# Performance work log

Hardware: AMD Instinct MI355X
Metric: run time of the kernel (lower is better)

Reference implementation:

```python
import jax, jax.numpy as jnp
import numpy as np

NL, D, DI, N, R, K = 4, 256, 512, 16, 16, 4  # layers, d_model, d_inner, d_state, dt_rank, conv kernel


def setup_inputs() -> dict:
    key = jax.random.key(0)
    ks = jax.random.split(key, 10)
    b, nc, nt = 8, 256, 64
    xc = jax.random.normal(ks[0], (b, nc, D), jnp.float32)
    xt = jax.random.normal(ks[1], (b, nt, D), jnp.float32)
    ln_g = jnp.ones((NL, D), jnp.float32)
    ln_b = jnp.zeros((NL, D), jnp.float32)
    W_in = jax.random.normal(ks[2], (NL, D, 2 * DI), jnp.float32) * (D ** -0.5)
    W_conv = jax.random.normal(ks[3], (NL, DI, 1, K), jnp.float32) * 0.2
    b_conv = jnp.zeros((NL, DI), jnp.float32)
    W_x = jax.random.normal(ks[4], (NL, DI, R + 2 * N), jnp.float32) * (DI ** -0.5)
    W_dt = jax.random.normal(ks[5], (NL, R, DI), jnp.float32) * (R ** -0.5)
    b_dt = jax.random.normal(ks[6], (NL, DI), jnp.float32) * 0.5 - 4.0  # softplus ~ 0.02
    A_log = jnp.broadcast_to(jnp.log(jnp.arange(1, N + 1, dtype=jnp.float32)), (NL, DI, N)).copy()
    Dp = jnp.ones((NL, DI), jnp.float32)
    W_out = jax.random.normal(ks[7], (NL, DI, D), jnp.float32) * (DI ** -0.5)
    return dict(xc=xc, xt=xt, ln_g=ln_g, ln_b=ln_b, W_in=W_in, W_conv=W_conv, b_conv=b_conv,
                W_x=W_x, W_dt=W_dt, b_dt=b_dt, A_log=A_log, Dp=Dp, W_out=W_out)


def _mamba_layer(x, g, beta, Wi, Wc, bc, Wx, Wdt, bdt, Alog, Dvec, Wo):
    # x: [B, L, D]; pre-LN residual Mamba-1 block
    mu = jnp.mean(x, axis=-1, keepdims=True)
    var = jnp.var(x, axis=-1, keepdims=True)
    h = (x - mu) * jax.lax.rsqrt(var + 1e-5) * g + beta
    xz = h @ Wi                              # [B, L, 2*DI]
    xp, z = xz[..., :DI], xz[..., DI:]
    # causal depthwise conv1d
    xcv = jax.lax.conv_general_dilated(xp.transpose(0, 2, 1), Wc, (1,), [(K - 1, 0)],
                                       feature_group_count=DI,
                                       dimension_numbers=('NCH', 'OIH', 'NCH'))
    xcv = jax.nn.silu(xcv.transpose(0, 2, 1) + bc)  # [B, L, DI]
    dbl = xcv @ Wx                           # [B, L, R+2N]
    dt = jax.nn.softplus(dbl[..., :R] @ Wdt + bdt)   # [B, L, DI]
    Bm = dbl[..., R:R + N]                   # [B, L, N]
    Cm = dbl[..., R + N:]                    # [B, L, N]
    A = -jnp.exp(Alog)                       # [DI, N]

    def step(hst, inp):
        x_t, dt_t, b_t, c_t = inp            # [B,DI],[B,DI],[B,N],[B,N]
        dA = jnp.exp(dt_t[:, :, None] * A)   # [B, DI, N]
        hst = dA * hst + (dt_t * x_t)[:, :, None] * b_t[:, None, :]
        return hst, jnp.einsum('bdn,bn->bd', hst, c_t)

    h0 = jnp.zeros((x.shape[0], DI, N), x.dtype)
    _, ys = jax.lax.scan(step, h0, (xcv.transpose(1, 0, 2), dt.transpose(1, 0, 2),
                                    Bm.transpose(1, 0, 2), Cm.transpose(1, 0, 2)))
    y = ys.transpose(1, 0, 2) + xcv * Dvec
    y = y * jax.nn.silu(z)
    return x + y @ Wo


def reference(xc, xt, ln_g, ln_b, W_in, W_conv, b_conv, W_x, W_dt, b_dt, A_log, Dp, W_out):
    b, nc, d = xc.shape
    nt = xt.shape[1]
    # replicate context per target token: [b*nt, nc+1, d]
    xr = jnp.broadcast_to(xc[:, None], (b, nt, nc, d)).reshape(b * nt, nc, d)
    x = jnp.concatenate([xr, xt.reshape(b * nt, 1, d)], axis=1)
    for i in range(NL):
        x = _mamba_layer(x, ln_g[i], ln_b[i], W_in[i], W_conv[i], b_conv[i],
                         W_x[i], W_dt[i], b_dt[i], A_log[i], Dp[i], W_out[i])
    return x[:, -1, :].reshape(b, nt, d)
```

## Files before the change

### kernel.cpp

```cpp
#include <hip/hip_runtime.h>
#include <hip/hip_bf16.h>

#define D_     256
#define TWO_DI 1024
#define DI_    512
#define NSTATE 16
#define RR     16
#define NDBL   48
#define BSEQ   8
#define NC     256
#define NCHUNK 16
#define CLEN   16
#define CTX    2048
#define TGT    512

typedef __attribute__((ext_vector_type(8))) short short8v;
typedef __attribute__((ext_vector_type(8))) unsigned short ushort8v;
typedef __attribute__((ext_vector_type(4))) float floatx4;

__device__ __forceinline__ float siluf(float x) { return x / (1.f + __expf(-x)); }
__device__ __forceinline__ float softplusf(float x) {
  return fmaxf(x, 0.f) + log1pf(__expf(-fabsf(x)));
}
__device__ __forceinline__ unsigned short f2bf(float x) {
  unsigned u = __float_as_uint(x);
  u += 0x7fffu + ((u >> 16) & 1u);
  return (unsigned short)(u >> 16);
}
__device__ __forceinline__ float bf2f(unsigned short b) {
  return __uint_as_float((unsigned)b << 16);
}

__global__ __launch_bounds__(256) void prep_all(
    const float* __restrict__ W_in, const float* __restrict__ W_o,
    const float* __restrict__ W_x, const float* __restrict__ Alog,
    const float* __restrict__ W_dt,
    unsigned short* __restrict__ Wint, unsigned short* __restrict__ Wot,
    unsigned short* __restrict__ Wxt, float* __restrict__ Aneg,
    float* __restrict__ WdtT)
{
  __shared__ float tile[32][33];
  int b = blockIdx.x;
  const float* src; unsigned short* dst; int R, C, cx, ry;
  if (b < 1024) {
    int z = b >> 8, t = b & 255; cx = t & 31; ry = t >> 5; R = 256; C = 1024;
    src = W_in + (size_t)z * R * C; dst = Wint + (size_t)z * R * C;
  } else if (b < 1536) {
    int bb = b - 1024; int z = bb >> 7, t = bb & 127; cx = t & 7; ry = t >> 3; R = 512; C = 256;
    src = W_o + (size_t)z * R * C; dst = Wot + (size_t)z * R * C;
  } else if (b < 1664) {
    int bb = b - 1536; int z = bb >> 5, t = bb & 31; cx = t & 1; ry = t >> 1; R = 512; C = 48;
    src = W_x + (size_t)z * R * C; dst = Wxt + (size_t)z * R * C;
  } else if (b < 1792) {
    int i = (b - 1664) * 256 + threadIdx.x;
    if (i < 4 * DI_ * NSTATE) Aneg[i] = -__expf(Alog[i]);
    return;
  } else {
    int i = (b - 1792) * 256 + threadIdx.x;
    int z = i >> 13, rem = i & 8191, c = rem >> 4, r = rem & 15;
    WdtT[i] = W_dt[(size_t)z * RR * DI_ + r * DI_ + c];
    return;
  }
  int c0 = cx * 32, r0 = ry * 32;
  int tx = threadIdx.x & 31, ty = threadIdx.x >> 5;
#pragma unroll
  for (int i = 0; i < 4; ++i) {
    int r = r0 + ty + i * 8;
    tile[ty + i * 8][tx] = (r < R && c0 + tx < C) ? src[(size_t)r * C + c0 + tx] : 0.f;
  }
  __syncthreads();
#pragma unroll
  for (int i = 0; i < 4; ++i) {
    int c = c0 + ty + i * 8;
    if (c < C && r0 + tx < R)
      dst[(size_t)c * R + r0 + tx] = f2bf(tile[tx][ty + i * 8]);
  }
}

template<int EPI>
__device__ __forceinline__ void gemm_in_ln_body(
    unsigned short (*As)[72], unsigned short (*Bs)[72],
    float* gs, float* bs, int bx, int by,
    const float* __restrict__ X, const float* __restrict__ g,
    const float* __restrict__ be, const unsigned short* __restrict__ Bt,
    float* __restrict__ C, int N,
    const float* __restrict__ cconv, const float* __restrict__ Wc4,
    unsigned short* __restrict__ xcv_bf, float* __restrict__ zbuf)
{
  const int K = D_;
  int tid = threadIdx.x;
  int n0 = bx * 64, m0 = by * 64;
  int w = tid >> 6, lane = tid & 63;
  int lr = lane & 15, kq = lane >> 4;
  int wr = w >> 1, wc = w & 1;
  int srow = tid >> 2, schunk = (tid & 3) * 16;
  const float* Apf = &X[(size_t)(m0 + srow) * K];
  {
    const float4* xr = reinterpret_cast<const float4*>(&Apf[(tid & 3) * 64]);
    float s = 0.f, sq = 0.f;
#pragma unroll
    for (int i = 0; i < 16; ++i) {
      float4 v = xr[i];
      s += v.x + v.y + v.z + v.w;
      sq += v.x * v.x + v.y * v.y + v.z * v.z + v.w * v.w;
    }
    s += __shfl_xor(s, 1);  s += __shfl_xor(s, 2);
    sq += __shfl_xor(sq, 1); sq += __shfl_xor(sq, 2);
    float mu = s * (1.f / K);
    float rstd = rsqrtf(sq * (1.f / K) - mu * mu + 1e-5f);
    gs[tid] = g[tid]; bs[tid] = be[tid];
    const unsigned short* Bp = &Bt[(size_t)(n0 + srow) * K + schunk];
    float4 af[4];
#pragma unroll
    for (int i = 0; i < 4; ++i)
      af[i] = *reinterpret_cast<const float4*>(&Apf[schunk + i * 4]);
    ushort8v b0 = *reinterpret_cast<const ushort8v*>(Bp);
    ushort8v b1 = *reinterpret_cast<const ushort8v*>(Bp + 8);
    floatx4 acc[2][2] = {};
    for (int k0 = 0; k0 < K; k0 += 64) {
      __syncthreads();
      {
        int cb = k0 + schunk;
        ushort8v o0, o1;
#pragma unroll
        for (int i = 0; i < 4; ++i) {
          float4 v = af[i];
          unsigned short e0 = f2bf((v.x - mu) * rstd * gs[cb + i * 4 + 0] + bs[cb + i * 4 + 0]);
          unsigned short e1 = f2bf((v.y - mu) * rstd * gs[cb + i * 4 + 1] + bs[cb + i * 4 + 1]);
          unsigned short e2 = f2bf((v.z - mu) * rstd * gs[cb + i * 4 + 2] + bs[cb + i * 4 + 2]);
          unsigned short e3 = f2bf((v.w - mu) * rstd * gs[cb + i * 4 + 3] + bs[cb + i * 4 + 3]);
          if (i < 2) { o0[i*4] = (short)e0; o0[i*4+1] = (short)e1; o0[i*4+2] = (short)e2; o0[i*4+3] = (short)e3; }
          else { int j = (i-2)*4; o1[j] = (short)e0; o1[j+1] = (short)e1; o1[j+2] = (short)e2; o1[j+3] = (short)e3; }
        }
        *reinterpret_cast<ushort8v*>(&As[srow][schunk])     = o0;
        *reinterpret_cast<ushort8v*>(&As[srow][schunk + 8]) = o1;
      }
      *reinterpret_cast<ushort8v*>(&Bs[srow][schunk])     = b0;
      *reinterpret_cast<ushort8v*>(&Bs[srow][schunk + 8]) = b1;
      __syncthreads();
      if (k0 + 64 < K) {
#pragma unroll
        for (int i = 0; i < 4; ++i)
          af[i] = *reinterpret_cast<const float4*>(&Apf[k0 + 64 + schunk + i * 4]);
        b0 = *reinterpret_cast<const ushort8v*>(Bp + k0 + 64);
        b1 = *reinterpret_cast<const ushort8v*>(Bp + k0 + 72);
      }
#pragma unroll
      for (int ks = 0; ks < 2; ++ks) {
        short8v af2[2], bf2v[2];
#pragma unroll
        for (int f = 0; f < 2; ++f)
          af2[f] = *reinterpret_cast<const short8v*>(&As[wr * 32 + f * 16 + lr][ks * 32 + kq * 8]);
#pragma unroll
        for (int g2 = 0; g2 < 2; ++g2)
          bf2v[g2] = *reinterpret_cast<const short8v*>(&Bs[wc * 32 + g2 * 16 + lr][ks * 32 + kq * 8]);
#pragma unroll
        for (int f = 0; f < 2; ++f)
#pragma unroll
          for (int g2 = 0; g2 < 2; ++g2)
            acc[f][g2] = __builtin_amdgcn_mfma_f32_16x16x32_bf16(af2[f], bf2v[g2], acc[f][g2], 0, 0, 0);
      }
    }
#pragma unroll
    for (int f = 0; f < 2; ++f)
#pragma unroll
      for (int g2 = 0; g2 < 2; ++g2) {
        int col = n0 + wc * 32 + g2 * 16 + lr;
#pragma unroll
        for (int r = 0; r < 4; ++r) {
          int row = m0 + wr * 32 + f * 16 + kq * 4 + r;
          float v = acc[f][g2][r];
          if (EPI == 0) {
            C[(size_t)row * N + col] = v;
          } else {
            int bb = row >> 6;
            if (col < DI_) {
              float sv = siluf(cconv[bb * DI_ + col] + v * Wc4[col * 4 + 3]);
              xcv_bf[(size_t)row * DI_ + col] = f2bf(sv);
            } else {
              zbuf[(size_t)row * DI_ + (col - DI_)] = v;
            }
          }
        }
      }
  }
}

template<int EPI>
__global__ __launch_bounds__(256) void gemm_in_ln(
    const float* __restrict__ X, const float* __restrict__ g,
    const float* __restrict__ be, const unsigned short* __restrict__ Bt,
    float* __restrict__ C,
    const float* __restrict__ cconv, const float* __restrict__ Wc4,
    unsigned short* __restrict__ xcv_bf, float* __restrict__ zbuf)
{
  __shared__ unsigned short As[64][72];
  __shared__ unsigned short Bs[64][72];
  __shared__ float gs[256], bs[256];
  gemm_in_ln_body<EPI>(As, Bs, gs, bs, blockIdx.x, blockIdx.y, X, g, be, Bt,
                       C, TWO_DI, cconv, Wc4, xcv_bf, zbuf);
}

__global__ __launch_bounds__(256) void fused_gemm_in_ln(
    const float* __restrict__ Xa, const float* __restrict__ ga,
    const float* __restrict__ ba, float* __restrict__ Ca,
    const unsigned short* __restrict__ Bta,
    const float* __restrict__ Xb, const float* __restrict__ gb,
    const float* __restrict__ bb, const unsigned short* __restrict__ Btb,
    const float* __restrict__ cconv, const float* __restrict__ Wc4,
    unsigned short* __restrict__ xcv_bf, float* __restrict__ zbuf)
{
  __shared__ unsigned short As[64][72];
  __shared__ unsigned short Bs[64][72];
  __shared__ float gs[256], bs[256];
  int f = blockIdx.x;
  if (f < 512)
    gemm_in_ln_body<0>(As, Bs, gs, bs, f & 15, f >> 4, Xa, ga, ba, Bta,
                       Ca, TWO_DI, nullptr, nullptr, nullptr, nullptr);
  else {
    f -= 512;
    gemm_in_ln_body<1>(As, Bs, gs, bs, f & 15, f >> 4, Xb, gb, bb, Btb,
                       nullptr, TWO_DI, cconv, Wc4, xcv_bf, zbuf);
  }
}

__global__ __launch_bounds__(256) void gemm_out(
    const unsigned short* __restrict__ A, const unsigned short* __restrict__ Bt,
    const float* __restrict__ resid, float* __restrict__ C, int N, int K)
{
  __shared__ unsigned short As[64][72];
  __shared__ unsigned short Bs[64][72];
  int tid = threadIdx.x;
  int n0 = blockIdx.x * 64, m0 = blockIdx.y * 64;
  int w = tid >> 6, lane = tid & 63;
  int lr = lane & 15, kq = lane >> 4;
  int wr = w >> 1, wc = w & 1;
  int srow = tid >> 2, schunk = (tid & 3) * 16;
  const unsigned short* Ap = &A[(size_t)(m0 + srow) * K + schunk];
  const unsigned short* Bp = &Bt[(size_t)(n0 + srow) * K + schunk];
  ushort8v a0 = *reinterpret_cast<const ushort8v*>(Ap);
  ushort8v a1 = *reinterpret_cast<const ushort8v*>(Ap + 8);
  ushort8v b0 = *reinterpret_cast<const ushort8v*>(Bp);
  ushort8v b1 = *reinterpret_cast<const ushort8v*>(Bp + 8);
  floatx4 acc[2][2] = {};
  for (int k0 = 0; k0 < K; k0 += 64) {
    __syncthreads();
    *reinterpret_cast<ushort8v*>(&As[srow][schunk])     = a0;
    *reinterpret_cast<ushort8v*>(&As[srow][schunk + 8]) = a1;
    *reinterpret_cast<ushort8v*>(&Bs[srow][schunk])     = b0;
    *reinterpret_cast<ushort8v*>(&Bs[srow][schunk + 8]) = b1;
    __syncthreads();
    if (k0 + 64 < K) {
      a0 = *reinterpret_cast<const ushort8v*>(Ap + k0 + 64);
      a1 = *reinterpret_cast<const ushort8v*>(Ap + k0 + 72);
      b0 = *reinterpret_cast<const ushort8v*>(Bp + k0 + 64);
      b1 = *reinterpret_cast<const ushort8v*>(Bp + k0 + 72);
    }
#pragma unroll
    for (int ks = 0; ks < 2; ++ks) {
      short8v af[2], bf2v[2];
#pragma unroll
      for (int f = 0; f < 2; ++f)
        af[f] = *reinterpret_cast<const short8v*>(&As[wr * 32 + f * 16 + lr][ks * 32 + kq * 8]);
#pragma unroll
      for (int g2 = 0; g2 < 2; ++g2)
        bf2v[g2] = *reinterpret_cast<const short8v*>(&Bs[wc * 32 + g2 * 16 + lr][ks * 32 + kq * 8]);
#pragma unroll
      for (int f = 0; f < 2; ++f)
#pragma unroll
        for (int g2 = 0; g2 < 2; ++g2)
          acc[f][g2] = __builtin_amdgcn_mfma_f32_16x16x32_bf16(af[f], bf2v[g2], acc[f][g2], 0, 0, 0);
    }
  }
#pragma unroll
  for (int f = 0; f < 2; ++f)
#pragma unroll
    for (int g2 = 0; g2 < 2; ++g2) {
      int col = n0 + wc * 32 + g2 * 16 + lr;
#pragma unroll
      for (int r = 0; r < 4; ++r) {
        int row = m0 + wr * 32 + f * 16 + kq * 4 + r;
        float v = acc[f][g2][r] + resid[(size_t)row * N + col];
        C[(size_t)row * N + col] = v;
      }
    }
}

__device__ __forceinline__ void gemm_s_body(int bx, int by,
    const unsigned short* __restrict__ A, const unsigned short* __restrict__ Bt,
    const float* __restrict__ resid, float* __restrict__ C, int N, int K)
{
  __shared__ unsigned short As[32][72];
  __shared__ unsigned short Bs[32][72];
  int tid = threadIdx.x;
  int n0 = bx * 32, m0 = by * 32;
  int w = tid >> 6, lane = tid & 63;
  int lr = lane & 15, kq = lane >> 4;
  int wr = w >> 1, wc = w & 1;
  int srow = tid >> 3, schunk = (tid & 7) * 8;
  const unsigned short* Ap = &A[(size_t)(m0 + srow) * K + schunk];
  const unsigned short* Bp = &Bt[(size_t)(n0 + srow) * K + schunk];
  ushort8v a0 = *reinterpret_cast<const ushort8v*>(Ap);
  ushort8v b0 = *reinterpret_cast<const ushort8v*>(Bp);
  floatx4 acc = {};
  for (int k0 = 0; k0 < K; k0 += 64) {
    __syncthreads();
    *reinterpret_cast<ushort8v*>(&As[srow][schunk]) = a0;
    *reinterpret_cast<ushort8v*>(&Bs[srow][schunk]) = b0;
    __syncthreads();
    if (k0 + 64 < K) {
      a0 = *reinterpret_cast<const ushort8v*>(Ap + k0 + 64);
      b0 = *reinterpret_cast<const ushort8v*>(Bp + k0 + 64);
    }
#pragma unroll
    for (int ks = 0; ks < 2; ++ks) {
      short8v af = *reinterpret_cast<const short8v*>(&As[wr * 16 + lr][ks * 32 + kq * 8]);
      short8v bf = *reinterpret_cast<const short8v*>(&Bs[wc * 16 + lr][ks * 32 + kq * 8]);
      acc = __builtin_amdgcn_mfma_f32_16x16x32_bf16(af, bf, acc, 0, 0, 0);
    }
  }
  int col = n0 + wc * 16 + lr;
#pragma unroll
  for (int r = 0; r < 4; ++r) {
    int row = m0 + wr * 16 + kq * 4 + r;
    float v = acc[r] + resid[(size_t)row * N + col];
    C[(size_t)row * N + col] = v;
  }
}

__global__ __launch_bounds__(256) void gemm_s(
    const unsigned short* __restrict__ A, const unsigned short* __restrict__ Bt,
    const float* __restrict__ resid, float* __restrict__ C, int N, int K)
{
  gemm_s_body(blockIdx.x, blockIdx.y, A, Bt, resid, C, N, K);
}

__device__ __forceinline__ void conv_body_lean(int blk,
    const float* __restrict__ xz, const float* __restrict__ Wc,
    const float* __restrict__ bc, const unsigned short* __restrict__ Wxt,
    const float* __restrict__ WdtT, const float* __restrict__ bdt,
    unsigned short* __restrict__ xcvb, float* __restrict__ dtb,
    float* __restrict__ dblg, float* __restrict__ cconv)
{
  __shared__ unsigned short xcs[16][528];
  __shared__ float dbl_s[16][48];
  int seq = blk >> 4, ch = blk & 15;
  int tok0 = blk * 16;
  int tid = threadIdx.x;
  int base = ch * 16;
#pragma unroll
  for (int hh = 0; hh < 2; ++hh) {
    int c = tid + hh * 256;
    const float4 wv = *reinterpret_cast<const float4*>(&Wc[c * 4]);
    float bcv = bc[c];
    const float* xzs = &xz[(size_t)(seq * NC) * TWO_DI + c];
    float r[19];
#pragma unroll
    for (int i = 0; i < 19; ++i) {
      int tl = base - 3 + i;
      r[i] = (tl >= 0) ? xzs[(size_t)tl * TWO_DI] : 0.f;
    }
#pragma unroll
    for (int t = 0; t < 16; ++t) {
      float acc = bcv + r[t] * wv.x + r[t + 1] * wv.y + r[t + 2] * wv.z + r[t + 3] * wv.w;
      unsigned short sv = f2bf(siluf(acc));
      xcs[t][c] = sv;
      xcvb[(size_t)(tok0 + t) * DI_ + c] = sv;
    }
    if (ch == 15)
      cconv[seq * DI_ + c] = bcv + r[16] * wv.x + r[17] * wv.y + r[18] * wv.z;
  }
  __syncthreads();
  int w = tid >> 6, lane = tid & 63, lr = lane & 15, kq = lane >> 4;
  if (w < 3) {
    floatx4 acc = {};
#pragma unroll
    for (int kc = 0; kc < 16; ++kc) {
      short8v bb = *reinterpret_cast<const short8v*>(&Wxt[(size_t)(w * 16 + lr) * DI_ + kc * 32 + kq * 8]);
      short8v aa = *reinterpret_cast<const short8v*>(&xcs[lr][kc * 32 + kq * 8]);
      acc = __builtin_amdgcn_mfma_f32_16x16x32_bf16(aa, bb, acc, 0, 0, 0);
    }
#pragma unroll
    for (int r2 = 0; r2 < 4; ++r2) {
      int t = kq * 4 + r2, col = w * 16 + lr;
      dbl_s[t][col] = acc[r2];
      dblg[(size_t)(tok0 + t) * NDBL + col] = acc[r2];
    }
  }
  __syncthreads();
#pragma unroll
  for (int hh = 0; hh < 2; ++hh) {
    int c = tid + hh * 256;
    float wr_[16];
    const float4* wt4 = reinterpret_cast<const float4*>(&WdtT[c * 16]);
#pragma unroll
    for (int q = 0; q < 4; ++q) {
      float4 v4 = wt4[q];
      wr_[q * 4] = v4.x; wr_[q * 4 + 1] = v4.y; wr_[q * 4 + 2] = v4.z; wr_[q * 4 + 3] = v4.w;
    }
    float bv = bdt[c];
#pragma unroll
    for (int t = 0; t < 16; ++t) {
      float accd = bv;
#pragma unroll
      for (int r2 = 0; r2 < 16; ++r2) accd += dbl_s[t][r2] * wr_[r2];
      dtb[(size_t)(tok0 + t) * DI_ + c] = softplusf(accd);
    }
  }
}

__global__ __launch_bounds__(256) void conv_lean_kern(
    const float* __restrict__ xz, const float* __restrict__ Wc,
    const float* __restrict__ bc, const unsigned short* __restrict__ Wxt,
    const float* __restrict__ WdtT, const float* __restrict__ bdt,
    unsigned short* __restrict__ xcvb, float* __restrict__ dtb,
    float* __restrict__ dblg, float* __restrict__ cconv)
{
  conv_body_lean(blockIdx.x, xz, Wc, bc, Wxt, WdtT, bdt, xcvb, dtb, dblg, cconv);
}

__device__ __forceinline__ void sp_body(int b,
    const float* __restrict__ dblg, const unsigned short* __restrict__ xcvb,
    const float* __restrict__ dtb, const float* __restrict__ Aneg,
    float* __restrict__ Sb, float* __restrict__ Pb)
{
  int dg = b & 31, sc = b >> 5;
  int tid = threadIdx.x;
  int tt = tid >> 4, cc = tid & 15;
  int tok0 = sc * CLEN;
  __shared__ float dts[16][17], xs[16][17], Bsh[16][17];
  dts[tt][cc] = dtb[(size_t)(tok0 + tt) * DI_ + dg * 16 + cc];
  xs[tt][cc]  = bf2f(xcvb[(size_t)(tok0 + tt) * DI_ + dg * 16 + cc]);
  Bsh[tt][cc] = dblg[(size_t)(tok0 + tt) * NDBL + RR + cc];
  __syncthreads();
  int dl = tt, n = cc;
  int d = dg * 16 + dl;
  float A = Aneg[d * NSTATE + n];
  float Bn[16];
#pragma unroll
  for (int t = 0; t < CLEN; ++t) Bn[t] = Bsh[t][n];
  float h = 0.f, p = 1.f;
#pragma unroll
  for (int t = 0; t < CLEN; ++t) {
    float dtv = dts[t][dl];
    float dA  = __expf(dtv * A);
    h = fmaf(dA, h, dtv * xs[t][dl] * Bn[t]);
    p *= dA;
  }
  size_t o = ((size_t)sc * DI_ + d) * NSTATE + n;
  Sb[o] = h; Pb[o] = p;
}

__global__ __launch_bounds__(256) void sp_kern(
    const float* __restrict__ dblg, const unsigned short* __restrict__ xcvb,
    const float* __restrict__ dtb, const float* __restrict__ Aneg,
    float* __restrict__ Sb, float* __restrict__ Pb)
{
  sp_body(blockIdx.x, dblg, xcvb, dtb, Aneg, Sb, Pb);
}

__global__ __launch_bounds__(256) void fused_sp_gout(
    const unsigned short* __restrict__ Ag, const unsigned short* __restrict__ Btg,
    const float* __restrict__ residg, float* __restrict__ Cg,
    const float* __restrict__ dblg, const unsigned short* __restrict__ xcvb,
    const float* __restrict__ dtb, const float* __restrict__ Aneg,
    float* __restrict__ Sb, float* __restrict__ Pb)
{
  if (blockIdx.x < 128) {
    int f = blockIdx.x;
    gemm_s_body(f & 7, f >> 3, Ag, Btg, residg, Cg, D_, DI_);
  } else {
    sp_body(blockIdx.x - 128, dblg, xcvb, dtb, Aneg, Sb, Pb);
  }
}

__global__ __launch_bounds__(256) void scan_fin(
    const float* __restrict__ dblg, const unsigned short* __restrict__ xcvb,
    const float* __restrict__ xz, const float* __restrict__ dtb,
    const float* __restrict__ Sb, const float* __restrict__ Pb,
    const float* __restrict__ Aneg, const float* __restrict__ Dp,
    unsigned short* __restrict__ yb, float* __restrict__ hstate)
{
  int b = blockIdx.x;
  int dg = b & 31, sc = b >> 5;
  int seq = sc >> 4, chunk = sc & 15;
  int tid = threadIdx.x;
  int tt = tid >> 4, cc = tid & 15;
  int tok0 = sc * CLEN;
  __shared__ float dts[16][17], xs[16][17], zs[16][17], Bsh[16][17], Csh[16][17], ys[16][17];
  dts[tt][cc] = dtb[(size_t)(tok0 + tt) * DI_ + dg * 16 + cc];
  xs[tt][cc]  = bf2f(xcvb[(size_t)(tok0 + tt) * DI_ + dg * 16 + cc]);
  zs[tt][cc]  = xz[(size_t)(tok0 + tt) * TWO_DI + DI_ + dg * 16 + cc];
  Bsh[tt][cc] = dblg[(size_t)(tok0 + tt) * NDBL + RR + cc];
  Csh[tt][cc] = dblg[(size_t)(tok0 + tt) * NDBL + RR + NSTATE + cc];
  __syncthreads();
  int dl = tt, n = cc;
  int d = dg * 16 + dl;
  float A  = Aneg[d * NSTATE + n];
  float Dv = Dp[d];
  float Bn[16], Cn[16];
#pragma unroll
  for (int t = 0; t < CLEN; ++t) { Bn[t] = Bsh[t][n]; Cn[t] = Csh[t][n]; }
  float h = 0.f;
  for (int c2 = 0; c2 < chunk; ++c2) {
    size_t o = ((size_t)(seq * NCHUNK + c2) * DI_ + d) * NSTATE + n;
    h = fmaf(Pb[o], h, Sb[o]);
  }
#pragma unroll
  for (int t = 0; t < CLEN; ++t) {
    float dtv = dts[t][dl];
    float xv  = xs[t][dl];
    float dA  = __expf(dtv * A);
    h = fmaf(dA, h, dtv * xv * Bn[t]);
    float p = h * Cn[t];
    p += __shfl_xor(p, 1); p += __shfl_xor(p, 2);
    p += __shfl_xor(p, 4); p += __shfl_xor(p, 8);
    if (n == 0) ys[t][dl] = (p + xv * Dv) * siluf(zs[t][dl]);
  }
  __syncthreads();
  yb[(size_t)(tok0 + tt) * DI_ + dg * 16 + cc] = f2bf(ys[tt][cc]);
  if (chunk == NCHUNK - 1)
    hstate[(size_t)seq * DI_ * NSTATE + d * NSTATE + n] = h;
}

__device__ __forceinline__ void ssm_body(int blk,
    const unsigned short* __restrict__ xcv_bf, const float* __restrict__ zbuf,
    const unsigned short* __restrict__ Wx, const float* __restrict__ WdtT_l,
    const float* __restrict__ bdt_l, const float* __restrict__ An_l,
    const float* __restrict__ Dp_l, const float* __restrict__ hs,
    unsigned short* __restrict__ ybf)
{
  __shared__ float dbl_s[16][48];
  int tg = blk >> 3, cg = blk & 7;
  int tok0 = tg * 16;
  int b = tg >> 2;
  int tid = threadIdx.x;
  int w = tid >> 6, lane = tid & 63, lr = lane & 15, kq = lane >> 4;
  if (w < 3) {
    floatx4 acc = {};
#pragma unroll
    for (int kc = 0; kc < 16; ++kc) {
      short8v bb = *reinterpret_cast<const short8v*>(&Wx[(size_t)(w * 16 + lr) * DI_ + kc * 32 + kq * 8]);
      short8v aa = *reinterpret_cast<const short8v*>(&xcv_bf[(size_t)(tok0 + lr) * DI_ + kc * 32 + kq * 8]);
      acc = __builtin_amdgcn_mfma_f32_16x16x32_bf16(aa, bb, acc, 0, 0, 0);
    }
#pragma unroll
    for (int r = 0; r < 4; ++r)
      dbl_s[kq * 4 + r][w * 16 + lr] = acc[r];
  }
  __syncthreads();
  int c = cg * 64 + (tid & 63);
  int t0 = (tid >> 6) * 4;
  float wdt_r[16], An[16], hr[16];
  const float4* wt4 = reinterpret_cast<const float4*>(&WdtT_l[c * 16]);
  const float4* An4 = reinterpret_cast<const float4*>(&An_l[c * NSTATE]);
  const float4* hr4 = reinterpret_cast<const float4*>(&hs[(size_t)b * DI_ * NSTATE + c * NSTATE]);
#pragma unroll
  for (int q = 0; q < 4; ++q) {
    float4 wv = wt4[q]; wdt_r[q*4]=wv.x; wdt_r[q*4+1]=wv.y; wdt_r[q*4+2]=wv.z; wdt_r[q*4+3]=wv.w;
    float4 a = An4[q]; An[q*4]=a.x; An[q*4+1]=a.y; An[q*4+2]=a.z; An[q*4+3]=a.w;
    float4 hv = hr4[q]; hr[q*4]=hv.x; hr[q*4+1]=hv.y; hr[q*4+2]=hv.z; hr[q*4+3]=hv.w;
  }
  float Dv = Dp_l[c], bv = bdt_l[c];
#pragma unroll
  for (int tt = 0; tt < 4; ++tt) {
    int t = t0 + tt;
    float accd = bv;
#pragma unroll
    for (int r = 0; r < 16; ++r) accd += dbl_s[t][r] * wdt_r[r];
    float dtv = softplusf(accd);
    float xv = bf2f(xcv_bf[(size_t)(tok0 + t) * DI_ + c]);
    float coef = dtv * xv;
    float y = 0.f;
#pragma unroll
    for (int n = 0; n < 16; ++n) {
      float hn = fmaf(__expf(dtv * An[n]), hr[n], coef * dbl_s[t][RR + n]);
      y = fmaf(hn, dbl_s[t][RR + NSTATE + n], y);
    }
    float yv = (y + xv * Dv) * siluf(zbuf[(size_t)(tok0 + t) * DI_ + c]);
    ybf[(size_t)(tok0 + t) * DI_ + c] = f2bf(yv);
  }
}

__global__ __launch_bounds__(256) void tgt_ssm2(
    const unsigned short* __restrict__ xcv_bf, const float* __restrict__ zbuf,
    const unsigned short* __restrict__ Wx, const float* __restrict__ WdtT_l,
    const float* __restrict__ bdt_l, const float* __restrict__ An_l,
    const float* __restrict__ Dp_l, const float* __restrict__ hs,
    unsigned short* __restrict__ ybf)
{
  ssm_body(blockIdx.x, xcv_bf, zbuf, Wx, WdtT_l, bdt_l, An_l, Dp_l, hs, ybf);
}

__global__ __launch_bounds__(256) void fused_conv_ssm(
    const float* __restrict__ xz, const float* __restrict__ Wc,
    const float* __restrict__ bc, const unsigned short* __restrict__ WxtA,
    const float* __restrict__ WdtTA, const float* __restrict__ bdtA,
    unsigned short* __restrict__ xcvb, float* __restrict__ dtb,
    float* __restrict__ dblg, float* __restrict__ cconv,
    const unsigned short* __restrict__ xcv_bfB, const float* __restrict__ zbufB,
    const unsigned short* __restrict__ WxB, const float* __restrict__ WdtTB,
    const float* __restrict__ bdtB, const float* __restrict__ AnB,
    const float* __restrict__ DpB, const float* __restrict__ hsB,
    unsigned short* __restrict__ ybfB)
{
  if (blockIdx.x < BSEQ * NCHUNK)
    conv_body_lean(blockIdx.x, xz, Wc, bc, WxtA, WdtTA, bdtA,
                   xcvb, dtb, dblg, cconv);
  else
    ssm_body(blockIdx.x - BSEQ * NCHUNK, xcv_bfB, zbufB, WxB, WdtTB, bdtB,
             AnB, DpB, hsB, ybfB);
}

extern "C" void kernel_launch(void* const* d_in, const int* in_sizes, int n_in,
                              void* d_out, int out_size, void* d_ws, size_t ws_size,
                              hipStream_t stream)
{
  const float* xc   = (const float*)d_in[0];
  const float* xt   = (const float*)d_in[1];
  const float* ln_g = (const float*)d_in[2];
  const float* ln_b = (const float*)d_in[3];
  const float* W_in = (const float*)d_in[4];
  const float* W_cv = (const float*)d_in[5];
  const float* b_cv = (const float*)d_in[6];
  const float* W_x  = (const float*)d_in[7];
  const float* W_dt = (const float*)d_in[8];
  const float* b_dt = (const float*)d_in[9];
  const float* Alog = (const float*)d_in[10];
  const float* Dp   = (const float*)d_in[11];
  const float* W_o  = (const float*)d_in[12];
  float* out = (float*)d_out;

  float* ws = (float*)d_ws;
  size_t off = 0;
  auto alloc = [&](size_t n) { float* p = ws + off; off += n; return p; };
  float* xz     = alloc((size_t)CTX * TWO_DI);
  float* dtb    = alloc((size_t)CTX * DI_);
  float* dblg   = alloc((size_t)CTX * NDBL);
  float* xcur   = alloc((size_t)CTX * D_);
  float* Sb     = alloc((size_t)BSEQ * NCHUNK * DI_ * NSTATE);
  float* Pb     = alloc((size_t)BSEQ * NCHUNK * DI_ * NSTATE);
  float* cconvT = alloc((size_t)4 * BSEQ * DI_);
  float* hst    = alloc((size_t)4 * BSEQ * DI_ * NSTATE);
  float* Aneg   = alloc((size_t)4 * DI_ * NSTATE);
  float* WdtT   = alloc((size_t)4 * DI_ * RR);
  float* zbufB  = alloc((size_t)TGT * DI_);
  float* xtb    = alloc((size_t)TGT * D_);
  unsigned short* xcvb    = (unsigned short*)alloc((size_t)CTX * DI_ / 2);
  unsigned short* yb_bf   = (unsigned short*)alloc((size_t)CTX * DI_ / 2);
  unsigned short* xcv_bfB = (unsigned short*)alloc((size_t)TGT * DI_ / 2);
  unsigned short* y_bfB   = (unsigned short*)alloc((size_t)TGT * DI_ / 2);
  unsigned short* Wint    = (unsigned short*)alloc((size_t)4 * TWO_DI * D_ / 2);
  unsigned short* Wot     = (unsigned short*)alloc((size_t)4 * D_ * DI_ / 2);
  unsigned short* Wxt     = (unsigned short*)alloc((size_t)4 * NDBL * DI_ / 2);
  if (off * sizeof(float) > ws_size) return;

  prep_all<<<1920, 256, 0, stream>>>(W_in, W_o, W_x, Alog, W_dt,
                                     Wint, Wot, Wxt, Aneg, WdtT);

  gemm_in_ln<0><<<dim3(16, CTX / 64), 256, 0, stream>>>(
      xc, ln_g, ln_b, Wint, xz, nullptr, nullptr, nullptr, nullptr);
  conv_lean_kern<<<BSEQ * NCHUNK, 256, 0, stream>>>(
      xz, W_cv, b_cv, Wxt, WdtT, b_dt, xcvb, dtb, dblg, cconvT);
  sp_kern<<<BSEQ * NCHUNK * 32, 256, 0, stream>>>(dblg, xcvb, dtb, Aneg, Sb, Pb);
  scan_fin<<<BSEQ * NCHUNK * 32, 256, 0, stream>>>(
      dblg, xcvb, xz, dtb, Sb, Pb, Aneg, Dp, yb_bf, hst);
  gemm_out<<<dim3(D_ / 64, CTX / 64), 256, 0, stream>>>(
      yb_bf, Wot, xc, xcur, D_, DI_);

  for (int l = 0; l < 3; ++l) {
    int la = l + 1;
    const float* xinB = (l == 0) ? xt : xtb;
    fused_gemm_in_ln<<<512 + 128, 256, 0, stream>>>(
        xcur, ln_g + la * D_, ln_b + la * D_, xz, Wint + (size_t)la * TWO_DI * D_,
        xinB, ln_g + l * D_, ln_b + l * D_, Wint + (size_t)l * TWO_DI * D_,
        cconvT + (size_t)l * BSEQ * DI_, W_cv + l * DI_ * 4, xcv_bfB, zbufB);
    fused_conv_ssm<<<BSEQ * NCHUNK + 256, 256, 0, stream>>>(
        xz, W_cv + la * DI_ * 4, b_cv + la * DI_, Wxt + (size_t)la * NDBL * DI_,
        WdtT + (size_t)la * DI_ * RR, b_dt + la * DI_,
        xcvb, dtb, dblg, cconvT + (size_t)la * BSEQ * DI_,
        xcv_bfB, zbufB, Wxt + (size_t)l * NDBL * DI_, WdtT + (size_t)l * DI_ * RR,
        b_dt + l * DI_, Aneg + l * DI_ * NSTATE, Dp + l * DI_,
        hst + (size_t)l * BSEQ * DI_ * NSTATE, y_bfB);
    fused_sp_gout<<<128 + BSEQ * NCHUNK * 32, 256, 0, stream>>>(
        y_bfB, Wot + (size_t)l * D_ * DI_, xinB, xtb,
        dblg, xcvb, dtb, Aneg + la * DI_ * NSTATE, Sb, Pb);
    scan_fin<<<BSEQ * NCHUNK * 32, 256, 0, stream>>>(
        dblg, xcvb, xz, dtb, Sb, Pb, Aneg + la * DI_ * NSTATE, Dp + la * DI_,
        yb_bf, hst + (size_t)la * BSEQ * DI_ * NSTATE);
    if (la < 3)
      gemm_out<<<dim3(D_ / 64, CTX / 64), 256, 0, stream>>>(
          yb_bf, Wot + (size_t)la * D_ * DI_, xcur, xcur, D_, DI_);
  }

  gemm_in_ln<1><<<dim3(16, TGT / 64), 256, 0, stream>>>(
      xtb, ln_g + 3 * D_, ln_b + 3 * D_, Wint + (size_t)3 * TWO_DI * D_, nullptr,
      cconvT + (size_t)3 * BSEQ * DI_, W_cv + 3 * DI_ * 4, xcv_bfB, zbufB);
  tgt_ssm2<<<256, 256, 0, stream>>>(xcv_bfB, zbufB,
      Wxt + (size_t)3 * NDBL * DI_, WdtT + (size_t)3 * DI_ * RR, b_dt + 3 * DI_,
      Aneg + 3 * DI_ * NSTATE, Dp + 3 * DI_,
      hst + (size_t)3 * BSEQ * DI_ * NSTATE, y_bfB);
  gemm_s<<<dim3(D_ / 32, TGT / 32), 256, 0, stream>>>(
      y_bfB, Wot + (size_t)3 * D_ * DI_, xtb, out, D_, DI_);
}
```

Before: 316.7 us.

## Fold LayerNorm into W_in and fuse chunk-scan partials into conv kernel

Folds the LayerNorm gain into the bf16 W_in weights during prep and precomputes per-column weight sums and bias projections. The input GEMM can then feed raw x as bf16 and apply the mean and rstd correction in the epilogue. The chunk-local scan (S/P partials) moves into the conv kernel, which removes the separate sp kernel and its reload of dt, x and B. The layer loop merges scan_fin with the output GEMM to save a launch. The cost is atomics in prep and a different bf16 rounding point: raw x is quantised before centring, which can lose precision when the row mean is large relative to the spread.

```diff
diff --git a/kernel.cpp b/kernel.cpp
--- a/kernel.cpp
+++ b/kernel.cpp
@@ -35,17 +35,48 @@
     const float* __restrict__ W_in, const float* __restrict__ W_o,
     const float* __restrict__ W_x, const float* __restrict__ Alog,
     const float* __restrict__ W_dt,
+    const float* __restrict__ ln_g, const float* __restrict__ ln_b,
     unsigned short* __restrict__ Wint, unsigned short* __restrict__ Wot,
     unsigned short* __restrict__ Wxt, float* __restrict__ Aneg,
-    float* __restrict__ WdtT)
+    float* __restrict__ WdtT, float* __restrict__ cs0, float* __restrict__ bW)
 {
   __shared__ float tile[32][33];
   int b = blockIdx.x;
+  int tx = threadIdx.x & 31, ty = threadIdx.x >> 5;
+  if (b < 1024) {
+    int z = b >> 8, t = b & 255; int cx = t & 31, ry = t >> 5;
+    const int R = 256, C = 1024;
+    const float* src = W_in + (size_t)z * R * C;
+    unsigned short* dst = Wint + (size_t)z * R * C;
+    int c0 = cx * 32, r0 = ry * 32;
+#pragma unroll
+    for (int i = 0; i < 4; ++i)
+      tile[ty + i * 8][tx] = src[(size_t)(r0 + ty + i * 8) * C + c0 + tx];
+    __syncthreads();
+    float gv  = ln_g[z * D_ + r0 + tx];
+    float bev = ln_b[z * D_ + r0 + tx];
+#pragma unroll
+    for (int i = 0; i < 4; ++i) {
+      int c = c0 + ty + i * 8;
+      float wv = tile[tx][ty + i * 8];
+      unsigned short h = f2bf(wv * gv);
+      dst[(size_t)c * R + r0 + tx] = h;
+      float cs = bf2f(h);
+      float bs = bev * wv;
+#pragma unroll
+      for (int off = 1; off <= 16; off <<= 1) {
+        cs += __shfl_xor(cs, off);
+        bs += __shfl_xor(bs, off);
+      }
+      if (tx == 0) {
+        atomicAdd(&cs0[z * TWO_DI + c], cs);
+        atomicAdd(&bW[z * TWO_DI + c], bs);
+      }
+    }
+    return;
+  }
   const float* src; unsigned short* dst; int R, C, cx, ry;
-  if (b < 1024) {
-    int z = b >> 8, t = b & 255; cx = t & 31; ry = t >> 5; R = 256; C = 1024;
-    src = W_in + (size_t)z * R * C; dst = Wint + (size_t)z * R * C;
-  } else if (b < 1536) {
+  if (b < 1536) {
     int bb = b - 1024; int z = bb >> 7, t = bb & 127; cx = t & 7; ry = t >> 3; R = 512; C = 256;
     src = W_o + (size_t)z * R * C; dst = Wot + (size_t)z * R * C;
   } else if (b < 1664) {
@@ -62,7 +93,6 @@
     return;
   }
   int c0 = cx * 32, r0 = ry * 32;
-  int tx = threadIdx.x & 31, ty = threadIdx.x >> 5;
 #pragma unroll
   for (int i = 0; i < 4; ++i) {
     int r = r0 + ty + i * 8;
@@ -80,147 +110,144 @@
 template<int EPI>
 __device__ __forceinline__ void gemm_in_ln_body(
     unsigned short (*As)[72], unsigned short (*Bs)[72],
-    float* gs, float* bs, int bx, int by,
-    const float* __restrict__ X, const float* __restrict__ g,
-    const float* __restrict__ be, const unsigned short* __restrict__ Bt,
-    float* __restrict__ C, int N,
+    float* mus, float* rstds, int bx, int by,
+    const float* __restrict__ X, const unsigned short* __restrict__ Bt,
+    const float* __restrict__ cs0, const float* __restrict__ bW,
+    float* __restrict__ C,
     const float* __restrict__ cconv, const float* __restrict__ Wc4,
     unsigned short* __restrict__ xcv_bf, float* __restrict__ zbuf)
 {
-  const int K = D_;
+  const int K = D_, N = TWO_DI;
   int tid = threadIdx.x;
   int n0 = bx * 64, m0 = by * 64;
   int w = tid >> 6, lane = tid & 63;
   int lr = lane & 15, kq = lane >> 4;
   int wr = w >> 1, wc = w & 1;
-  int srow = tid >> 2, schunk = (tid & 3) * 16;
+  int srow = tid >> 2, q = tid & 3, schunk = q * 16;
   const float* Apf = &X[(size_t)(m0 + srow) * K];
-  {
-    const float4* xr = reinterpret_cast<const float4*>(&Apf[(tid & 3) * 64]);
-    float s = 0.f, sq = 0.f;
-#pragma unroll
-    for (int i = 0; i < 16; ++i) {
-      float4 v = xr[i];
-      s += v.x + v.y + v.z + v.w;
+  float4 xr[4][4];
+#pragma unroll
+  for (int j = 0; j < 4; ++j)
+#pragma unroll
+    for (int i = 0; i < 4; ++i)
+      xr[j][i] = *reinterpret_cast<const float4*>(&Apf[j * 64 + schunk + i * 4]);
+  float s = 0.f, sq = 0.f;
+#pragma unroll
+  for (int j = 0; j < 4; ++j)
+#pragma unroll
+    for (int i = 0; i < 4; ++i) {
+      float4 v = xr[j][i];
+      s  += v.x + v.y + v.z + v.w;
       sq += v.x * v.x + v.y * v.y + v.z * v.z + v.w * v.w;
     }
-    s += __shfl_xor(s, 1);  s += __shfl_xor(s, 2);
-    sq += __shfl_xor(sq, 1); sq += __shfl_xor(sq, 2);
-    float mu = s * (1.f / K);
-    float rstd = rsqrtf(sq * (1.f / K) - mu * mu + 1e-5f);
-    gs[tid] = g[tid]; bs[tid] = be[tid];
-    const unsigned short* Bp = &Bt[(size_t)(n0 + srow) * K + schunk];
-    float4 af[4];
-#pragma unroll
-    for (int i = 0; i < 4; ++i)
-      af[i] = *reinterpret_cast<const float4*>(&Apf[schunk + i * 4]);
-    ushort8v b0 = *reinterpret_cast<const ushort8v*>(Bp);
-    ushort8v b1 = *reinterpret_cast<const ushort8v*>(Bp + 8);
-    floatx4 acc[2][2] = {};
-    for (int k0 = 0; k0 < K; k0 += 64) {
-      __syncthreads();
-      {
-        int cb = k0 + schunk;
-        ushort8v o0, o1;
-#pragma unroll
-        for (int i = 0; i < 4; ++i) {
-          float4 v = af[i];
-          unsigned short e0 = f2bf((v.x - mu) * rstd * gs[cb + i * 4 + 0] + bs[cb + i * 4 + 0]);
-          unsigned short e1 = f2bf((v.y - mu) * rstd * gs[cb + i * 4 + 1] + bs[cb + i * 4 + 1]);
-          unsigned short e2 = f2bf((v.z - mu) * rstd * gs[cb + i * 4 + 2] + bs[cb + i * 4 + 2]);
-          unsigned short e3 = f2bf((v.w - mu) * rstd * gs[cb + i * 4 + 3] + bs[cb + i * 4 + 3]);
-          if (i < 2) { o0[i*4] = (short)e0; o0[i*4+1] = (short)e1; o0[i*4+2] = (short)e2; o0[i*4+3] = (short)e3; }
-          else { int j = (i-2)*4; o1[j] = (short)e0; o1[j+1] = (short)e1; o1[j+2] = (short)e2; o1[j+3] = (short)e3; }
-        }
-        *reinterpret_cast<ushort8v*>(&As[srow][schunk])     = o0;
-        *reinterpret_cast<ushort8v*>(&As[srow][schunk + 8]) = o1;
+  s += __shfl_xor(s, 1);  s += __shfl_xor(s, 2);
+  sq += __shfl_xor(sq, 1); sq += __shfl_xor(sq, 2);
+  float mu   = s * (1.f / K);
+  float rstd = rsqrtf(sq * (1.f / K) - mu * mu + 1e-5f);
+  if (q == 0) { mus[srow] = mu; rstds[srow] = rstd; }
+  const unsigned short* Bp = &Bt[(size_t)(n0 + srow) * K + schunk];
+  ushort8v b0 = *reinterpret_cast<const ushort8v*>(Bp);
+  ushort8v b1 = *reinterpret_cast<const ushort8v*>(Bp + 8);
+  floatx4 acc[2][2] = {};
+#pragma unroll
+  for (int j = 0; j < 4; ++j) {
+    __syncthreads();
+    {
+      ushort8v o0, o1;
+#pragma unroll
+      for (int i = 0; i < 4; ++i) {
+        float4 v = xr[j][i];
+        unsigned short e0 = f2bf(v.x), e1 = f2bf(v.y), e2 = f2bf(v.z), e3 = f2bf(v.w);
+        if (i < 2) { o0[i*4] = (short)e0; o0[i*4+1] = (short)e1; o0[i*4+2] = (short)e2; o0[i*4+3] = (short)e3; }
+        else { int jj = (i - 2) * 4; o1[jj] = (short)e0; o1[jj+1] = (short)e1; o1[jj+2] = (short)e2; o1[jj+3] = (short)e3; }
       }
-      *reinterpret_cast<ushort8v*>(&Bs[srow][schunk])     = b0;
-      *reinterpret_cast<ushort8v*>(&Bs[srow][schunk + 8]) = b1;
-      __syncthreads();
-      if (k0 + 64 < K) {
-#pragma unroll
-        for (int i = 0; i < 4; ++i)
-          af[i] = *reinterpret_cast<const float4*>(&Apf[k0 + 64 + schunk + i * 4]);
-        b0 = *reinterpret_cast<const ushort8v*>(Bp + k0 + 64);
-        b1 = *reinterpret_cast<const ushort8v*>(Bp + k0 + 72);
-      }
-#pragma unroll
-      for (int ks = 0; ks < 2; ++ks) {
-        short8v af2[2], bf2v[2];
-#pragma unroll
-        for (int f = 0; f < 2; ++f)
-          af2[f] = *reinterpret_cast<const short8v*>(&As[wr * 32 + f * 16 + lr][ks * 32 + kq * 8]);
+      *reinterpret_cast<ushort8v*>(&As[srow][schunk])     = o0;
+      *reinterpret_cast<ushort8v*>(&As[srow][schunk + 8]) = o1;
+    }
+    *reinterpret_cast<ushort8v*>(&Bs[srow][schunk])     = b0;
+    *reinterpret_cast<ushort8v*>(&Bs[srow][schunk + 8]) = b1;
+    __syncthreads();
+    if (j < 3) {
+      b0 = *reinterpret_cast<const ushort8v*>(Bp + j * 64 + 64);
+      b1 = *reinterpret_cast<const ushort8v*>(Bp + j * 64 + 72);
+    }
+#pragma unroll
+    for (int ks = 0; ks < 2; ++ks) {
+      short8v af2[2], bf2v[2];
+#pragma unroll
+      for (int f = 0; f < 2; ++f)
+        af2[f] = *reinterpret_cast<const short8v*>(&As[wr * 32 + f * 16 + lr][ks * 32 + kq * 8]);
+#pragma unroll
+      for (int g2 = 0; g2 < 2; ++g2)
+        bf2v[g2] = *reinterpret_cast<const short8v*>(&Bs[wc * 32 + g2 * 16 + lr][ks * 32 + kq * 8]);
+#pragma unroll
+      for (int f = 0; f < 2; ++f)
 #pragma unroll
         for (int g2 = 0; g2 < 2; ++g2)
-          bf2v[g2] = *reinterpret_cast<const short8v*>(&Bs[wc * 32 + g2 * 16 + lr][ks * 32 + kq * 8]);
-#pragma unroll
-        for (int f = 0; f < 2; ++f)
-#pragma unroll
-          for (int g2 = 0; g2 < 2; ++g2)
-            acc[f][g2] = __builtin_amdgcn_mfma_f32_16x16x32_bf16(af2[f], bf2v[g2], acc[f][g2], 0, 0, 0);
-      }
-    }
-#pragma unroll
-    for (int f = 0; f < 2; ++f)
-#pragma unroll
-      for (int g2 = 0; g2 < 2; ++g2) {
-        int col = n0 + wc * 32 + g2 * 16 + lr;
-#pragma unroll
-        for (int r = 0; r < 4; ++r) {
-          int row = m0 + wr * 32 + f * 16 + kq * 4 + r;
-          float v = acc[f][g2][r];
-          if (EPI == 0) {
-            C[(size_t)row * N + col] = v;
+          acc[f][g2] = __builtin_amdgcn_mfma_f32_16x16x32_bf16(af2[f], bf2v[g2], acc[f][g2], 0, 0, 0);
+    }
+  }
+#pragma unroll
+  for (int f = 0; f < 2; ++f)
+#pragma unroll
+    for (int g2 = 0; g2 < 2; ++g2) {
+      int col = n0 + wc * 32 + g2 * 16 + lr;
+      float c0v = cs0[col], bwv = bW[col];
+#pragma unroll
+      for (int r = 0; r < 4; ++r) {
+        int rowl = wr * 32 + f * 16 + kq * 4 + r;
+        int row  = m0 + rowl;
+        float v = rstds[rowl] * (acc[f][g2][r] - mus[rowl] * c0v) + bwv;
+        if (EPI == 0) {
+          C[(size_t)row * N + col] = v;
+        } else {
+          int bb = row >> 6;
+          if (col < DI_) {
+            float sv = siluf(cconv[bb * DI_ + col] + v * Wc4[col * 4 + 3]);
+            xcv_bf[(size_t)row * DI_ + col] = f2bf(sv);
           } else {
-            int bb = row >> 6;
-            if (col < DI_) {
-              float sv = siluf(cconv[bb * DI_ + col] + v * Wc4[col * 4 + 3]);
-              xcv_bf[(size_t)row * DI_ + col] = f2bf(sv);
-            } else {
-              zbuf[(size_t)row * DI_ + (col - DI_)] = v;
-            }
+            zbuf[(size_t)row * DI_ + (col - DI_)] = v;
           }
         }
       }
-  }
+    }
 }
 
 template<int EPI>
 __global__ __launch_bounds__(256) void gemm_in_ln(
-    const float* __restrict__ X, const float* __restrict__ g,
-    const float* __restrict__ be, const unsigned short* __restrict__ Bt,
+    const float* __restrict__ X, const unsigned short* __restrict__ Bt,
+    const float* __restrict__ cs0, const float* __restrict__ bW,
     float* __restrict__ C,
     const float* __restrict__ cconv, const float* __restrict__ Wc4,
     unsigned short* __restrict__ xcv_bf, float* __restrict__ zbuf)
 {
   __shared__ unsigned short As[64][72];
   __shared__ unsigned short Bs[64][72];
-  __shared__ float gs[256], bs[256];
-  gemm_in_ln_body<EPI>(As, Bs, gs, bs, blockIdx.x, blockIdx.y, X, g, be, Bt,
-                       C, TWO_DI, cconv, Wc4, xcv_bf, zbuf);
+  __shared__ float mus[64], rstds[64];
+  gemm_in_ln_body<EPI>(As, Bs, mus, rstds, blockIdx.x, blockIdx.y,
+                       X, Bt, cs0, bW, C, cconv, Wc4, xcv_bf, zbuf);
 }
 
 __global__ __launch_bounds__(256) void fused_gemm_in_ln(
-    const float* __restrict__ Xa, const float* __restrict__ ga,
-    const float* __restrict__ ba, float* __restrict__ Ca,
-    const unsigned short* __restrict__ Bta,
-    const float* __restrict__ Xb, const float* __restrict__ gb,
-    const float* __restrict__ bb, const unsigned short* __restrict__ Btb,
+    const float* __restrict__ Xa, const unsigned short* __restrict__ Bta,
+    const float* __restrict__ cs0a, const float* __restrict__ bWa,
+    float* __restrict__ Ca,
+    const float* __restrict__ Xb, const unsigned short* __restrict__ Btb,
+    const float* __restrict__ cs0b, const float* __restrict__ bWb,
     const float* __restrict__ cconv, const float* __restrict__ Wc4,
     unsigned short* __restrict__ xcv_bf, float* __restrict__ zbuf)
 {
   __shared__ unsigned short As[64][72];
   __shared__ unsigned short Bs[64][72];
-  __shared__ float gs[256], bs[256];
+  __shared__ float mus[64], rstds[64];
   int f = blockIdx.x;
   if (f < 512)
-    gemm_in_ln_body<0>(As, Bs, gs, bs, f & 15, f >> 4, Xa, ga, ba, Bta,
-                       Ca, TWO_DI, nullptr, nullptr, nullptr, nullptr);
+    gemm_in_ln_body<0>(As, Bs, mus, rstds, f & 15, f >> 4, Xa, Bta, cs0a, bWa,
+                       Ca, nullptr, nullptr, nullptr, nullptr);
   else {
     f -= 512;
-    gemm_in_ln_body<1>(As, Bs, gs, bs, f & 15, f >> 4, Xb, gb, bb, Btb,
-                       nullptr, TWO_DI, cconv, Wc4, xcv_bf, zbuf);
+    gemm_in_ln_body<1>(As, Bs, mus, rstds, f & 15, f >> 4, Xb, Btb, cs0b, bWb,
+                       nullptr, cconv, Wc4, xcv_bf, zbuf);
   }
 }
 
@@ -335,12 +362,14 @@
   gemm_s_body(blockIdx.x, blockIdx.y, A, Bt, resid, C, N, K);
 }
 
-__device__ __forceinline__ void conv_body_lean(int blk,
+__device__ __forceinline__ void conv_sp_body(int blk,
     const float* __restrict__ xz, const float* __restrict__ Wc,
     const float* __restrict__ bc, const unsigned short* __restrict__ Wxt,
     const float* __restrict__ WdtT, const float* __restrict__ bdt,
+    const float* __restrict__ Aneg,
     unsigned short* __restrict__ xcvb, float* __restrict__ dtb,
-    float* __restrict__ dblg, float* __restrict__ cconv)
+    float* __restrict__ dblg, float* __restrict__ cconv,
+    float* __restrict__ Sb, float* __restrict__ Pb)
 {
   __shared__ unsigned short xcs[16][528];
   __shared__ float dbl_s[16][48];
@@ -348,6 +377,7 @@
   int tok0 = blk * 16;
   int tid = threadIdx.x;
   int base = ch * 16;
+  float xv_t[2][16], dt_t[2][16];
 #pragma unroll
   for (int hh = 0; hh < 2; ++hh) {
     int c = tid + hh * 256;
@@ -362,10 +392,11 @@
     }
 #pragma unroll
     for (int t = 0; t < 16; ++t) {
-      float acc = bcv + r[t] * wv.x + r[t + 1] * wv.y + r[t + 2] * wv.z + r[t + 3] * wv.w;
-      unsigned short sv = f2bf(siluf(acc));
+      float a = bcv + r[t] * wv.x + r[t + 1] * wv.y + r[t + 2] * wv.z + r[t + 3] * wv.w;
+      unsigned short sv = f2bf(siluf(a));
       xcs[t][c] = sv;
       xcvb[(size_t)(tok0 + t) * DI_ + c] = sv;
+      xv_t[hh][t] = bf2f(sv);
     }
     if (ch == 15)
       cconv[seq * DI_ + c] = bcv + r[16] * wv.x + r[17] * wv.y + r[18] * wv.z;
@@ -394,9 +425,9 @@
     float wr_[16];
     const float4* wt4 = reinterpret_cast<const float4*>(&WdtT[c * 16]);
 #pragma unroll
-    for (int q = 0; q < 4; ++q) {
-      float4 v4 = wt4[q];
-      wr_[q * 4] = v4.x; wr_[q * 4 + 1] = v4.y; wr_[q * 4 + 2] = v4.z; wr_[q * 4 + 3] = v4.w;
+    for (int qq = 0; qq < 4; ++qq) {
+      float4 v4 = wt4[qq];
+      wr_[qq * 4] = v4.x; wr_[qq * 4 + 1] = v4.y; wr_[qq * 4 + 2] = v4.z; wr_[qq * 4 + 3] = v4.w;
     }
     float bv = bdt[c];
 #pragma unroll
@@ -404,84 +435,72 @@
       float accd = bv;
 #pragma unroll
       for (int r2 = 0; r2 < 16; ++r2) accd += dbl_s[t][r2] * wr_[r2];
-      dtb[(size_t)(tok0 + t) * DI_ + c] = softplusf(accd);
-    }
-  }
-}
-
-__global__ __launch_bounds__(256) void conv_lean_kern(
+      float dtv = softplusf(accd);
+      dt_t[hh][t] = dtv;
+      dtb[(size_t)(tok0 + t) * DI_ + c] = dtv;
+    }
+  }
+#pragma unroll
+  for (int hh = 0; hh < 2; ++hh) {
+    int d = tid + hh * 256;
+    float An[16];
+    const float4* An4 = reinterpret_cast<const float4*>(&Aneg[d * NSTATE]);
+#pragma unroll
+    for (int qq = 0; qq < 4; ++qq) {
+      float4 a = An4[qq];
+      An[qq * 4] = a.x; An[qq * 4 + 1] = a.y; An[qq * 4 + 2] = a.z; An[qq * 4 + 3] = a.w;
+    }
+    float h_n[16], p_n[16];
+#pragma unroll
+    for (int n = 0; n < 16; ++n) { h_n[n] = 0.f; p_n[n] = 1.f; }
+#pragma unroll
+    for (int t = 0; t < 16; ++t) {
+      float dtv  = dt_t[hh][t];
+      float coef = dtv * xv_t[hh][t];
+      float4 B0 = *reinterpret_cast<const float4*>(&dbl_s[t][RR]);
+      float4 B1 = *reinterpret_cast<const float4*>(&dbl_s[t][RR + 4]);
+      float4 B2 = *reinterpret_cast<const float4*>(&dbl_s[t][RR + 8]);
+      float4 B3 = *reinterpret_cast<const float4*>(&dbl_s[t][RR + 12]);
+      float Bv[16] = {B0.x, B0.y, B0.z, B0.w, B1.x, B1.y, B1.z, B1.w,
+                      B2.x, B2.y, B2.z, B2.w, B3.x, B3.y, B3.z, B3.w};
+#pragma unroll
+      for (int n = 0; n < 16; ++n) {
+        float dA = __expf(dtv * An[n]);
+        h_n[n] = fmaf(dA, h_n[n], coef * Bv[n]);
+        p_n[n] *= dA;
+      }
+    }
+    size_t ob = ((size_t)blk * DI_ + d) * NSTATE;
+#pragma unroll
+    for (int qq = 0; qq < 4; ++qq) {
+      *reinterpret_cast<float4*>(&Sb[ob + qq * 4]) =
+          make_float4(h_n[qq*4], h_n[qq*4+1], h_n[qq*4+2], h_n[qq*4+3]);
+      *reinterpret_cast<float4*>(&Pb[ob + qq * 4]) =
+          make_float4(p_n[qq*4], p_n[qq*4+1], p_n[qq*4+2], p_n[qq*4+3]);
+    }
+  }
+}
+
+__global__ __launch_bounds__(256) void conv_sp_kern(
     const float* __restrict__ xz, const float* __restrict__ Wc,
     const float* __restrict__ bc, const unsigned short* __restrict__ Wxt,
     const float* __restrict__ WdtT, const float* __restrict__ bdt,
+    const float* __restrict__ Aneg,
     unsigned short* __restrict__ xcvb, float* __restrict__ dtb,
-    float* __restrict__ dblg, float* __restrict__ cconv)
-{
-  conv_body_lean(blockIdx.x, xz, Wc, bc, Wxt, WdtT, bdt, xcvb, dtb, dblg, cconv);
-}
-
-__device__ __forceinline__ void sp_body(int b,
-    const float* __restrict__ dblg, const unsigned short* __restrict__ xcvb,
-    const float* __restrict__ dtb, const float* __restrict__ Aneg,
+    float* __restrict__ dblg, float* __restrict__ cconv,
     float* __restrict__ Sb, float* __restrict__ Pb)
 {
-  int dg = b & 31, sc = b >> 5;
-  int tid = threadIdx.x;
-  int tt = tid >> 4, cc = tid & 15;
-  int tok0 = sc * CLEN;
-  __shared__ float dts[16][17], xs[16][17], Bsh[16][17];
-  dts[tt][cc] = dtb[(size_t)(tok0 + tt) * DI_ + dg * 16 + cc];
-  xs[tt][cc]  = bf2f(xcvb[(size_t)(tok0 + tt) * DI_ + dg * 16 + cc]);
-  Bsh[tt][cc] = dblg[(size_t)(tok0 + tt) * NDBL + RR + cc];
-  __syncthreads();
-  int dl = tt, n = cc;
-  int d = dg * 16 + dl;
-  float A = Aneg[d * NSTATE + n];
-  float Bn[16];
-#pragma unroll
-  for (int t = 0; t < CLEN; ++t) Bn[t] = Bsh[t][n];
-  float h = 0.f, p = 1.f;
-#pragma unroll
-  for (int t = 0; t < CLEN; ++t) {
-    float dtv = dts[t][dl];
-    float dA  = __expf(dtv * A);
-    h = fmaf(dA, h, dtv * xs[t][dl] * Bn[t]);
-    p *= dA;
-  }
-  size_t o = ((size_t)sc * DI_ + d) * NSTATE + n;
-  Sb[o] = h; Pb[o] = p;
-}
-
-__global__ __launch_bounds__(256) void sp_kern(
-    const float* __restrict__ dblg, const unsigned short* __restrict__ xcvb,
-    const float* __restrict__ dtb, const float* __restrict__ Aneg,
-    float* __restrict__ Sb, float* __restrict__ Pb)
-{
-  sp_body(blockIdx.x, dblg, xcvb, dtb, Aneg, Sb, Pb);
-}
-
-__global__ __launch_bounds__(256) void fused_sp_gout(
-    const unsigned short* __restrict__ Ag, const unsigned short* __restrict__ Btg,
-    const float* __restrict__ residg, float* __restrict__ Cg,
-    const float* __restrict__ dblg, const unsigned short* __restrict__ xcvb,
-    const float* __restrict__ dtb, const float* __restrict__ Aneg,
-    float* __restrict__ Sb, float* __restrict__ Pb)
-{
-  if (blockIdx.x < 128) {
-    int f = blockIdx.x;
-    gemm_s_body(f & 7, f >> 3, Ag, Btg, residg, Cg, D_, DI_);
-  } else {
-    sp_body(blockIdx.x - 128, dblg, xcvb, dtb, Aneg, Sb, Pb);
-  }
-}
-
-__global__ __launch_bounds__(256) void scan_fin(
+  conv_sp_body(blockIdx.x, xz, Wc, bc, Wxt, WdtT, bdt, Aneg,
+               xcvb, dtb, dblg, cconv, Sb, Pb);
+}
+
+__device__ __forceinline__ void sf_body(int b,
     const float* __restrict__ dblg, const unsigned short* __restrict__ xcvb,
     const float* __restrict__ xz, const float* __restrict__ dtb,
     const float* __restrict__ Sb, const float* __restrict__ Pb,
     const float* __restrict__ Aneg, const float* __restrict__ Dp,
     unsigned short* __restrict__ yb, float* __restrict__ hstate)
 {
-  int b = blockIdx.x;
   int dg = b & 31, sc = b >> 5;
   int seq = sc >> 4, chunk = sc & 15;
   int tid = threadIdx.x;
@@ -523,6 +542,33 @@
     hstate[(size_t)seq * DI_ * NSTATE + d * NSTATE + n] = h;
 }
 
+__global__ __launch_bounds__(256) void scan_fin(
+    const float* __restrict__ dblg, const unsigned short* __restrict__ xcvb,
+    const float* __restrict__ xz, const float* __restrict__ dtb,
+    const float* __restrict__ Sb, const float* __restrict__ Pb,
+    const float* __restrict__ Aneg, const float* __restrict__ Dp,
+    unsigned short* __restrict__ yb, float* __restrict__ hstate)
+{
+  sf_body(blockIdx.x, dblg, xcvb, xz, dtb, Sb, Pb, Aneg, Dp, yb, hstate);
+}
+
+__global__ __launch_bounds__(256) void fused_fin_gout(
+    const unsigned short* __restrict__ Ag, const unsigned short* __restrict__ Btg,
+    const float* __restrict__ residg, float* __restrict__ Cg,
+    const float* __restrict__ dblg, const unsigned short* __restrict__ xcvb,
+    const float* __restrict__ xz, const float* __restrict__ dtb,
+    const float* __restrict__ Sb, const float* __restrict__ Pb,
+    const float* __restrict__ Aneg, const float* __restrict__ Dp,
+    unsigned short* __restrict__ yb, float* __restrict__ hstate)
+{
+  if (blockIdx.x < 128) {
+    int f = blockIdx.x;
+    gemm_s_body(f & 7, f >> 3, Ag, Btg, residg, Cg, D_, DI_);
+  } else {
+    sf_body(blockIdx.x - 128, dblg, xcvb, xz, dtb, Sb, Pb, Aneg, Dp, yb, hstate);
+  }
+}
+
 __device__ __forceinline__ void ssm_body(int blk,
     const unsigned short* __restrict__ xcv_bf, const float* __restrict__ zbuf,
     const unsigned short* __restrict__ Wx, const float* __restrict__ WdtT_l,
@@ -556,10 +602,10 @@
   const float4* An4 = reinterpret_cast<const float4*>(&An_l[c * NSTATE]);
   const float4* hr4 = reinterpret_cast<const float4*>(&hs[(size_t)b * DI_ * NSTATE + c * NSTATE]);
 #pragma unroll
-  for (int q = 0; q < 4; ++q) {
-    float4 wv = wt4[q]; wdt_r[q*4]=wv.x; wdt_r[q*4+1]=wv.y; wdt_r[q*4+2]=wv.z; wdt_r[q*4+3]=wv.w;
-    float4 a = An4[q]; An[q*4]=a.x; An[q*4+1]=a.y; An[q*4+2]=a.z; An[q*4+3]=a.w;
-    float4 hv = hr4[q]; hr[q*4]=hv.x; hr[q*4+1]=hv.y; hr[q*4+2]=hv.z; hr[q*4+3]=hv.w;
+  for (int qq = 0; qq < 4; ++qq) {
+    float4 wv = wt4[qq]; wdt_r[qq*4]=wv.x; wdt_r[qq*4+1]=wv.y; wdt_r[qq*4+2]=wv.z; wdt_r[qq*4+3]=wv.w;
+    float4 a = An4[qq]; An[qq*4]=a.x; An[qq*4+1]=a.y; An[qq*4+2]=a.z; An[qq*4+3]=a.w;
+    float4 hv = hr4[qq]; hr[qq*4]=hv.x; hr[qq*4+1]=hv.y; hr[qq*4+2]=hv.z; hr[qq*4+3]=hv.w;
   }
   float Dv = Dp_l[c], bv = bdt_l[c];
 #pragma unroll
@@ -592,12 +638,14 @@
   ssm_body(blockIdx.x, xcv_bf, zbuf, Wx, WdtT_l, bdt_l, An_l, Dp_l, hs, ybf);
 }
 
-__global__ __launch_bounds__(256) void fused_conv_ssm(
+__global__ __launch_bounds__(256) void fused_convsp_ssm(
     const float* __restrict__ xz, const float* __restrict__ Wc,
     const float* __restrict__ bc, const unsigned short* __restrict__ WxtA,
     const float* __restrict__ WdtTA, const float* __restrict__ bdtA,
+    const float* __restrict__ AnegA,
     unsigned short* __restrict__ xcvb, float* __restrict__ dtb,
     float* __restrict__ dblg, float* __restrict__ cconv,
+    float* __restrict__ Sb, float* __restrict__ Pb,
     const unsigned short* __restrict__ xcv_bfB, const float* __restrict__ zbufB,
     const unsigned short* __restrict__ WxB, const float* __restrict__ WdtTB,
     const float* __restrict__ bdtB, const float* __restrict__ AnB,
@@ -605,8 +653,8 @@
     unsigned short* __restrict__ ybfB)
 {
   if (blockIdx.x < BSEQ * NCHUNK)
-    conv_body_lean(blockIdx.x, xz, Wc, bc, WxtA, WdtTA, bdtA,
-                   xcvb, dtb, dblg, cconv);
+    conv_sp_body(blockIdx.x, xz, Wc, bc, WxtA, WdtTA, bdtA, AnegA,
+                 xcvb, dtb, dblg, cconv, Sb, Pb);
   else
     ssm_body(blockIdx.x - BSEQ * NCHUNK, xcv_bfB, zbufB, WxB, WdtTB, bdtB,
              AnB, DpB, hsB, ybfB);
@@ -644,6 +692,8 @@
   float* hst    = alloc((size_t)4 * BSEQ * DI_ * NSTATE);
   float* Aneg   = alloc((size_t)4 * DI_ * NSTATE);
   float* WdtT   = alloc((size_t)4 * DI_ * RR);
+  float* cs0b   = alloc((size_t)4 * TWO_DI);
+  float* bWb    = alloc((size_t)4 * TWO_DI);
   float* zbufB  = alloc((size_t)TGT * DI_);
   float* xtb    = alloc((size_t)TGT * D_);
   unsigned short* xcvb    = (unsigned short*)alloc((size_t)CTX * DI_ / 2);
@@ -655,14 +705,14 @@
   unsigned short* Wxt     = (unsigned short*)alloc((size_t)4 * NDBL * DI_ / 2);
   if (off * sizeof(float) > ws_size) return;
 
-  prep_all<<<1920, 256, 0, stream>>>(W_in, W_o, W_x, Alog, W_dt,
-                                     Wint, Wot, Wxt, Aneg, WdtT);
+  hipMemsetAsync(cs0b, 0, (size_t)8 * TWO_DI * sizeof(float), stream);
+  prep_all<<<1920, 256, 0, stream>>>(W_in, W_o, W_x, Alog, W_dt, ln_g, ln_b,
+                                     Wint, Wot, Wxt, Aneg, WdtT, cs0b, bWb);
 
   gemm_in_ln<0><<<dim3(16, CTX / 64), 256, 0, stream>>>(
-      xc, ln_g, ln_b, Wint, xz, nullptr, nullptr, nullptr, nullptr);
-  conv_lean_kern<<<BSEQ * NCHUNK, 256, 0, stream>>>(
-      xz, W_cv, b_cv, Wxt, WdtT, b_dt, xcvb, dtb, dblg, cconvT);
-  sp_kern<<<BSEQ * NCHUNK * 32, 256, 0, stream>>>(dblg, xcvb, dtb, Aneg, Sb, Pb);
+      xc, Wint, cs0b, bWb, xz, nullptr, nullptr, nullptr, nullptr);
+  conv_sp_kern<<<BSEQ * NCHUNK, 256, 0, stream>>>(
+      xz, W_cv, b_cv, Wxt, WdtT, b_dt, Aneg, xcvb, dtb, dblg, cconvT, Sb, Pb);
   scan_fin<<<BSEQ * NCHUNK * 32, 256, 0, stream>>>(
       dblg, xcvb, xz, dtb, Sb, Pb, Aneg, Dp, yb_bf, hst);
   gemm_out<<<dim3(D_ / 64, CTX / 64), 256, 0, stream>>>(
@@ -672,20 +722,18 @@
     int la = l + 1;
     const float* xinB = (l == 0) ? xt : xtb;
     fused_gemm_in_ln<<<512 + 128, 256, 0, stream>>>(
-        xcur, ln_g + la * D_, ln_b + la * D_, xz, Wint + (size_t)la * TWO_DI * D_,
-        xinB, ln_g + l * D_, ln_b + l * D_, Wint + (size_t)l * TWO_DI * D_,
+        xcur, Wint + (size_t)la * TWO_DI * D_, cs0b + la * TWO_DI, bWb + la * TWO_DI, xz,
+        xinB, Wint + (size_t)l * TWO_DI * D_, cs0b + l * TWO_DI, bWb + l * TWO_DI,
         cconvT + (size_t)l * BSEQ * DI_, W_cv + l * DI_ * 4, xcv_bfB, zbufB);
-    fused_conv_ssm<<<BSEQ * NCHUNK + 256, 256, 0, stream>>>(
+    fused_convsp_ssm<<<BSEQ * NCHUNK + 256, 256, 0, stream>>>(
         xz, W_cv + la * DI_ * 4, b_cv + la * DI_, Wxt + (size_t)la * NDBL * DI_,
-        WdtT + (size_t)la * DI_ * RR, b_dt + la * DI_,
-        xcvb, dtb, dblg, cconvT + (size_t)la * BSEQ * DI_,
+        WdtT + (size_t)la * DI_ * RR, b_dt + la * DI_, Aneg + la * DI_ * NSTATE,
+        xcvb, dtb, dblg, cconvT + (size_t)la * BSEQ * DI_, Sb, Pb,
         xcv_bfB, zbufB, Wxt + (size_t)l * NDBL * DI_, WdtT + (size_t)l * DI_ * RR,
         b_dt + l * DI_, Aneg + l * DI_ * NSTATE, Dp + l * DI_,
         hst + (size_t)l * BSEQ * DI_ * NSTATE, y_bfB);
-    fused_sp_gout<<<128 + BSEQ * NCHUNK * 32, 256, 0, stream>>>(
+    fused_fin_gout<<<128 + BSEQ * NCHUNK * 32, 256, 0, stream>>>(
         y_bfB, Wot + (size_t)l * D_ * DI_, xinB, xtb,
-        dblg, xcvb, dtb, Aneg + la * DI_ * NSTATE, Sb, Pb);
-    scan_fin<<<BSEQ * NCHUNK * 32, 256, 0, stream>>>(
         dblg, xcvb, xz, dtb, Sb, Pb, Aneg + la * DI_ * NSTATE, Dp + la * DI_,
         yb_bf, hst + (size_t)la * BSEQ * DI_ * NSTATE);
     if (la < 3)
@@ -694,7 +742,7 @@
   }
 
   gemm_in_ln<1><<<dim3(16, TGT / 64), 256, 0, stream>>>(
-      xtb, ln_g + 3 * D_, ln_b + 3 * D_, Wint + (size_t)3 * TWO_DI * D_, nullptr,
+      xtb, Wint + (size_t)3 * TWO_DI * D_, cs0b + 3 * TWO_DI, bWb + 3 * TWO_DI, nullptr,
       cconvT + (size_t)3 * BSEQ * DI_, W_cv + 3 * DI_ * 4, xcv_bfB, zbufB);
   tgt_ssm2<<<256, 256, 0, stream>>>(xcv_bfB, zbufB,
       Wxt + (size_t)3 * NDBL * DI_, WdtT + (size_t)3 * DI_ * RR, b_dt + 3 * DI_,
```

Measured after the change: 337.0 us. +6.4%, slower.
